# Performance work log

Hardware: AMD Instinct MI355X
Metric: run time of the kernel (lower is better)

Reference implementation:

```python
import jax, jax.numpy as jnp
import numpy as np

HID = 16; HEADS = 8; NB_IN = 8; NB_OUT = 128
B = 128; NPG = 512; N = B * NPG; DEG = 16; E = N * DEG


def _gatv2(x, src, dst, wl, bl, wr, br, att, bias, heads, ch, concat):
    n = x.shape[0]
    xl = (x @ wl + bl).reshape(n, heads, ch)  # source transform
    xr = (x @ wr + br).reshape(n, heads, ch)  # target transform
    e = jax.nn.leaky_relu(xl[src] + xr[dst], negative_slope=0.2)  # [E,H,C]
    logits = jnp.einsum('ehc,hc->eh', e, att)  # [E,H]
    m = jax.ops.segment_max(logits, dst, num_segments=n)
    m = jnp.where(jnp.isfinite(m), m, 0.0)  # guard empty segments
    a = jnp.exp(logits - m[dst])
    denom = jax.ops.segment_sum(a, dst, num_segments=n)
    alpha = a / (denom[dst] + 1e-16)  # segment softmax over incoming edges
    out = jax.ops.segment_sum(alpha[:, :, None] * xl[src], dst, num_segments=n)  # [N,H,C]
    out = out.reshape(n, heads * ch) if concat else out.mean(axis=1)
    return out + bias


def setup_inputs() -> dict:
    key = jax.random.key(0)
    ks = jax.random.split(key, 24)
    x = jax.random.normal(ks[0], (N, NB_IN), jnp.float32)
    # within-graph random edges: local ids + graph offsets
    eg = jax.random.randint(ks[1], (2, B, NPG * DEG), 0, NPG)
    off = (jnp.arange(B) * NPG)[None, :, None]
    edge_index = (eg + off).reshape(2, -1).astype(jnp.int64)
    batch = (jnp.arange(N) // NPG).astype(jnp.int64)
    w = lambda k, i, o: jax.random.normal(k, (i, o), jnp.float32) * (1.0 / np.sqrt(i))
    return {
        'x': x, 'edge_index': edge_index, 'batch': batch,
        'w1l': w(ks[2], NB_IN, HID * HEADS), 'b1l': jnp.zeros(HID * HEADS),
        'w1r': w(ks[3], NB_IN, HID * HEADS), 'b1r': jnp.zeros(HID * HEADS),
        'att1': jax.random.normal(ks[4], (HEADS, HID), jnp.float32) * 0.25,
        'bias1': jnp.zeros(HID * HEADS),
        'w2l': w(ks[5], HID * HEADS, HID * HEADS), 'b2l': jnp.zeros(HID * HEADS),
        'w2r': w(ks[6], HID * HEADS, HID * HEADS), 'b2r': jnp.zeros(HID * HEADS),
        'att2': jax.random.normal(ks[7], (HEADS, HID), jnp.float32) * 0.25,
        'bias2': jnp.zeros(HID * HEADS),
        'w3l': w(ks[8], HID * HEADS, NB_OUT), 'b3l': jnp.zeros(NB_OUT),
        'w3r': w(ks[9], HID * HEADS, NB_OUT), 'b3r': jnp.zeros(NB_OUT),
        'att3': jax.random.normal(ks[10], (1, NB_OUT), jnp.float32) * 0.1,
        'bias3': jnp.zeros(NB_OUT),
        'wh': w(ks[11], NB_OUT * 4, NB_OUT), 'bh': jnp.zeros(NB_OUT),
    }


def reference(x, edge_index, batch, w1l, b1l, w1r, b1r, att1, bias1,
              w2l, b2l, w2r, b2r, att2, bias2,
              w3l, b3l, w3r, b3r, att3, bias3, wh, bh):
    src, dst = edge_index[0], edge_index[1]
    h = _gatv2(x, src, dst, w1l, b1l, w1r, b1r, att1, bias1, HEADS, HID, True)
    h = jax.nn.leaky_relu(h, negative_slope=0.01)
    h = _gatv2(h, src, dst, w2l, b2l, w2r, b2r, att2, bias2, HEADS, HID, True)
    h = jax.nn.leaky_relu(h, negative_slope=0.01)
    h = _gatv2(h, src, dst, w3l, b3l, w3r, b3r, att3, bias3, 1, NB_OUT, False)
    # global pooling: min, max, mean, sum per graph
    s = jax.ops.segment_sum(h, batch, num_segments=B)
    cnt = jax.ops.segment_sum(jnp.ones((N, 1), h.dtype), batch, num_segments=B)
    pooled = jnp.concatenate([
        jax.ops.segment_min(h, batch, num_segments=B),
        jax.ops.segment_max(h, batch, num_segments=B),
        s / jnp.maximum(cnt, 1.0),
        s,
    ], axis=1)  # [B, 4*NB_OUT]
    return jax.nn.leaky_relu(pooled, negative_slope=0.01) @ wh + bh
```

## Files before the change

kernel.cpp:

```cpp
#include <hip/hip_runtime.h>
#include <hip/hip_bf16.h>

typedef __hip_bfloat16 bf16;


__device__ __forceinline__ float bf2f(unsigned int u16) {
    union { unsigned int i; float f; } c; c.i = u16 << 16; return c.f;
}

__device__ __forceinline__ float v9_ldb(const float* p, long i) { return p[i]; }
__device__ __forceinline__ float v9_ldb(const bf16* p, long i) {
    return __bfloat162float(p[i]);
}
__device__ __forceinline__ void v9_stb(float* p, long i, float v) { p[i] = v; }
__device__ __forceinline__ void v9_stb(bf16* p, long i, float v) {
    p[i] = __float2bfloat16(v);
}
__device__ __forceinline__ float2 v11_ld2(const float* p, unsigned i) {
    return *(const float2*)(p + i);
}
__device__ __forceinline__ float2 v11_ld2(const bf16* p, unsigned i) {
    const unsigned u = *(const unsigned*)(p + i);
    float2 r; r.x = bf2f(u & 0xFFFFu); r.y = bf2f(u >> 16); return r;
}
__device__ __forceinline__ float v9_ldin(const void* p, long i, int f32) {
    if (f32) return ((const float*)p)[i];
    return __bfloat162float(((const bf16*)p)[i]);
}

extern "C" __global__ void v9_detect(const unsigned short* xw, const unsigned int* ew,
                                     int* flg) {
    __shared__ int cp, cz;
    if (threadIdx.x == 0) { cp = 0; cz = 0; }
    __syncthreads();
    int lp = 0, lz = 0;
    for (int t = threadIdx.x; t < 1024; t += blockDim.x) {
        unsigned short u = xw[2 * t];
        int e = (u >> 7) & 0xFF;
        if ((e >= 100 && e <= 140) || u == 0) lp++;
        if (ew[2 * t + 1] == 0u) lz++;
    }
    atomicAdd(&cp, lp); atomicAdd(&cz, lz);
    __syncthreads();
    if (threadIdx.x == 0) {
        flg[0] = (cp < 700) ? 1 : 0;
        flg[1] = (cz > 512) ? 1 : 0;
    }
}

__device__ __forceinline__ void v9_edge(const void* ei, int E, int e, int i64,
                                        int& s, int& d) {
    if (i64) {
        const long long* p = (const long long*)ei;
        s = (int)p[e]; d = (int)p[E + e];
    } else {
        const int* p = (const int*)ei;
        s = p[e]; d = p[E + e];
    }
}

extern "C" __global__ void v9_zero(int* cnt, int n) {
    int i = blockIdx.x * blockDim.x + threadIdx.x;
    if (i < n) cnt[i] = 0;
}

extern "C" __global__ void v9_count(const void* ei, int E, int* cnt, int n,
                                    const int* flg) {
    int e = blockIdx.x * blockDim.x + threadIdx.x;
    if (e >= E) return;
    int s, d; v9_edge(ei, E, e, flg[1], s, d);
    if ((unsigned)s >= (unsigned)n || (unsigned)d >= (unsigned)n) return;
    atomicAdd(&cnt[d], 1);
}

extern "C" __global__ __launch_bounds__(1024) void v9_scan(const int* cnt, int* off,
                                                           int n) {
    __shared__ int ls[1024];
    const int t = threadIdx.x;
    const int chunk = (n + 1023) / 1024;
    const int base = t * chunk;
    int s = 0;
    for (int i = base; i < base + chunk; ++i)
        if (i < n) s += cnt[i];
    ls[t] = s;
    __syncthreads();
    for (int d = 1; d < 1024; d <<= 1) {
        int o = (t >= d) ? ls[t - d] : 0;
        __syncthreads();
        ls[t] += o;
        __syncthreads();
    }
    int run = ls[t] - s;
    for (int i = base; i < base + chunk; ++i)
        if (i < n) { off[i] = run; run += cnt[i]; }
    if (t == 1023) off[n] = run;
}

extern "C" __global__ void v9_curinit(const int* off, int* cur, int n) {
    int i = blockIdx.x * blockDim.x + threadIdx.x;
    if (i < n) cur[i] = off[i];
}

extern "C" __global__ void v9_scatter(const void* ei, int E, int* cur, int* csr,
                                      int n, const int* flg) {
    int e = blockIdx.x * blockDim.x + threadIdx.x;
    if (e >= E) return;
    int s, d; v9_edge(ei, E, e, flg[1], s, d);
    if ((unsigned)s >= (unsigned)n || (unsigned)d >= (unsigned)n) return;
    int pos = atomicAdd(&cur[d], 1);
    if (pos >= 0 && pos < E) csr[pos] = s;
}

extern "C" __global__ void v13_sortseg(const int* __restrict__ off,
                                       int* __restrict__ csr, int n) {
    const int i = blockIdx.x * blockDim.x + threadIdx.x;
    if (i >= n) return;
    const int s0 = off[i], s1 = off[i + 1];
    for (int a = s0 + 1; a < s1; ++a) {
        const int v = csr[a];
        int b = a - 1;
        while (b >= s0 && csr[b] > v) { csr[b + 1] = csr[b]; --b; }
        csr[b + 1] = v;
    }
}

template <typename TB>
__global__ __launch_bounds__(256) void v11_gemm8d(const void* in,
        const void* wl, const void* bl, const void* wr, const void* br,
        TB* outl, TB* outr, int n, const int* flg) {
    __shared__ float sWl[8][128], sWr[8][128];
    __shared__ float sBl[128], sBr[128];
    __shared__ float sX[16][8];
    const int t = threadIdx.x;
    const int f = flg[0];
    for (int i = t; i < 1024; i += 256) {
        sWl[i >> 7][i & 127] = v9_ldin(wl, i, f);
        sWr[i >> 7][i & 127] = v9_ldin(wr, i, f);
    }
    if (t < 128) { sBl[t] = v9_ldin(bl, t, f); sBr[t] = v9_ldin(br, t, f); }
    const int nb = blockIdx.x * 16;
    if (t < 128) {
        const int node = nb + (t >> 3);
        if (node < n) sX[t >> 3][t & 7] = v9_ldin(in, (long)node * 8 + (t & 7), f);
    }
    __syncthreads();
    const int j = t & 127;
    const int g = t >> 7;
    float accl[8], accr[8];
#pragma unroll
    for (int q = 0; q < 8; ++q) { accl[q] = sBl[j]; accr[q] = sBr[j]; }
#pragma unroll
    for (int k = 0; k < 8; ++k) {
        const float wlv = sWl[k][j], wrv = sWr[k][j];
#pragma unroll
        for (int q = 0; q < 8; ++q) {
            const float xv = sX[g * 8 + q][k];
            accl[q] = fmaf(xv, wlv, accl[q]);
            accr[q] = fmaf(xv, wrv, accr[q]);
        }
    }
#pragma unroll
    for (int q = 0; q < 8; ++q) {
        const long node = nb + g * 8 + q;
        if (node < n) {
            v9_stb(outl, node * 128 + j, accl[q]);
            v9_stb(outr, node * 128 + j, accr[q]);
        }
    }
}

template <typename TB>
__global__ __launch_bounds__(512) void v10_gemm128(const TB* in, const void* w,
                                                   const void* b, TB* out, int n,
                                                   const int* flg) {
    __shared__ float sW[64 * 128];
    __shared__ float sX[64][64];
    const int t = threadIdx.x;
    const int f = flg[0];
    const int tx = t & 15;
    const int ty = t >> 4;
    const int n0 = ty * 2, n1 = n0 + 1;
    const int s0 = (n0 & 7) << 2, s1 = (n1 & 7) << 2;
    const long nbase = (long)blockIdx.x * 64;

    float bj[8];
#pragma unroll
    for (int j = 0; j < 8; ++j) bj[j] = v9_ldin(b, tx * 8 + j, f);

    float acc[16];
#pragma unroll
    for (int i = 0; i < 16; ++i) acc[i] = 0.f;

    for (int kk = 0; kk < 128; kk += 64) {
        __syncthreads();
        if (f) {
            const float4* ws = (const float4*)w + kk * 32;
#pragma unroll
            for (int i = 0; i < 4; ++i) {
                const int c = i * 512 + t;
                *(float4*)&sW[c * 4] = ws[c];
            }
        } else {
            const ushort4* ws = (const ushort4*)w + kk * 32;
#pragma unroll
            for (int i = 0; i < 4; ++i) {
                const int c = i * 512 + t;
                const ushort4 v = ws[c];
                float4 o;
                o.x = bf2f(v.x); o.y = bf2f(v.y); o.z = bf2f(v.z); o.w = bf2f(v.w);
                *(float4*)&sW[c * 4] = o;
            }
        }
#pragma unroll
        for (int i = 0; i < 2; ++i) {
            const int c = i * 512 + t;
            const int node = c >> 4;
            const int k0 = (c & 15) * 4;
            const long g = nbase + node;
            float4 v;
            if (g < n) {
                if constexpr (sizeof(TB) == 4) {
                    v = *(const float4*)((const float*)in + g * 128 + kk + k0);
                } else {
                    const ushort4 u = *(const ushort4*)((const bf16*)in + g * 128 + kk + k0);
                    v.x = bf2f(u.x); v.y = bf2f(u.y); v.z = bf2f(u.z); v.w = bf2f(u.w);
                }
            } else {
                v.x = v.y = v.z = v.w = 0.f;
            }
            *(float4*)&sX[node][k0 ^ ((node & 7) << 2)] = v;
        }
        __syncthreads();
#pragma unroll 4
        for (int k = 0; k < 64; ++k) {
            const float4 w0 = *(const float4*)&sW[k * 128 + tx * 8];
            const float4 w1 = *(const float4*)&sW[k * 128 + tx * 8 + 4];
            const float x0 = sX[n0][k ^ s0];
            const float x1 = sX[n1][k ^ s1];
            acc[0] = fmaf(x0, w0.x, acc[0]);
            acc[1] = fmaf(x0, w0.y, acc[1]);
            acc[2] = fmaf(x0, w0.z, acc[2]);
            acc[3] = fmaf(x0, w0.w, acc[3]);
            acc[4] = fmaf(x0, w1.x, acc[4]);
            acc[5] = fmaf(x0, w1.y, acc[5]);
            acc[6] = fmaf(x0, w1.z, acc[6]);
            acc[7] = fmaf(x0, w1.w, acc[7]);
            acc[8]  = fmaf(x1, w0.x, acc[8]);
            acc[9]  = fmaf(x1, w0.y, acc[9]);
            acc[10] = fmaf(x1, w0.z, acc[10]);
            acc[11] = fmaf(x1, w0.w, acc[11]);
            acc[12] = fmaf(x1, w1.x, acc[12]);
            acc[13] = fmaf(x1, w1.y, acc[13]);
            acc[14] = fmaf(x1, w1.z, acc[14]);
            acc[15] = fmaf(x1, w1.w, acc[15]);
        }
    }
    const long g0 = nbase + n0, g1 = nbase + n1;
    if (g0 < n) {
        if constexpr (sizeof(TB) == 4) {
            float4 o0 = {acc[0] + bj[0], acc[1] + bj[1], acc[2] + bj[2], acc[3] + bj[3]};
            float4 o1 = {acc[4] + bj[4], acc[5] + bj[5], acc[6] + bj[6], acc[7] + bj[7]};
            *(float4*)((float*)out + g0 * 128 + tx * 8)     = o0;
            *(float4*)((float*)out + g0 * 128 + tx * 8 + 4) = o1;
        } else {
#pragma unroll
            for (int j = 0; j < 8; ++j)
                v9_stb(out, g0 * 128 + tx * 8 + j, acc[j] + bj[j]);
        }
    }
    if (g1 < n) {
        if constexpr (sizeof(TB) == 4) {
            float4 o0 = {acc[8] + bj[0], acc[9] + bj[1], acc[10] + bj[2], acc[11] + bj[3]};
            float4 o1 = {acc[12] + bj[4], acc[13] + bj[5], acc[14] + bj[6], acc[15] + bj[7]};
            *(float4*)((float*)out + g1 * 128 + tx * 8)     = o0;
            *(float4*)((float*)out + g1 * 128 + tx * 8 + 4) = o1;
        } else {
#pragma unroll
            for (int j = 0; j < 8; ++j)
                v9_stb(out, g1 * 128 + tx * 8 + j, acc[8 + j] + bj[j]);
        }
    }
}

__device__ __forceinline__ float v12_logit(float2 xrv, float2 v, float a0, float a1) {
    float e0 = xrv.x + v.x; e0 = e0 > 0.f ? e0 : 0.2f * e0;
    float e1 = xrv.y + v.y; e1 = e1 > 0.f ? e1 : 0.2f * e1;
    return fmaf(e0, a0, e1 * a1);
}

template <typename TB, int LPG>
__global__ __launch_bounds__(256) void v12_agg(const TB* xl, const TB* xr,
                                               const int* csr, const int* off,
                                               const void* att, const void* bias,
                                               TB* out, int n, int E, int act,
                                               const int* flg) {
    const int node = blockIdx.x * 4 + (threadIdx.x >> 6);
    if (node >= n) return;
    const int lane = threadIdx.x & 63;
    const unsigned c0 = (unsigned)lane * 2;
    const int f = flg[0];
    const float2 xrv = v11_ld2(xr, (unsigned)node * 128u + c0);
    const float a0 = v9_ldin(att, c0, f), a1 = v9_ldin(att, c0 + 1, f);
    int s0 = off[node], s1 = off[node + 1];
    s0 = s0 < 0 ? 0 : (s0 > E ? E : s0);
    s1 = s1 < s0 ? s0 : (s1 > E ? E : s1);
    float m = -3.4e38f, den = 0.f, acc0 = 0.f, acc1 = 0.f;
    int i = s0;
    for (; i + 4 <= s1; i += 4) {
        const unsigned sA = (unsigned)csr[i];
        const unsigned sB = (unsigned)csr[i + 1];
        const unsigned sC = (unsigned)csr[i + 2];
        const unsigned sD = (unsigned)csr[i + 3];
        const float2 vA = v11_ld2(xl, sA * 128u + c0);
        const float2 vB = v11_ld2(xl, sB * 128u + c0);
        const float2 vC = v11_ld2(xl, sC * 128u + c0);
        const float2 vD = v11_ld2(xl, sD * 128u + c0);
        float pA = v12_logit(xrv, vA, a0, a1);
        float pB = v12_logit(xrv, vB, a0, a1);
        float pC = v12_logit(xrv, vC, a0, a1);
        float pD = v12_logit(xrv, vD, a0, a1);
#pragma unroll
        for (int o = 1; o < LPG; o <<= 1) {
            pA += __shfl_xor(pA, o);
            pB += __shfl_xor(pB, o);
            pC += __shfl_xor(pC, o);
            pD += __shfl_xor(pD, o);
        }
        const float bm = fmaxf(fmaxf(pA, pB), fmaxf(pC, pD));
        const float mn = fmaxf(m, bm);
        const float sc = __expf(m - mn);
        const float wA = __expf(pA - mn);
        const float wB = __expf(pB - mn);
        const float wC = __expf(pC - mn);
        const float wD = __expf(pD - mn);
        den  = fmaf(den, sc, (wA + wB) + (wC + wD));
        acc0 = fmaf(acc0, sc,
                    fmaf(wA, vA.x, fmaf(wB, vB.x, fmaf(wC, vC.x, wD * vD.x))));
        acc1 = fmaf(acc1, sc,
                    fmaf(wA, vA.y, fmaf(wB, vB.y, fmaf(wC, vC.y, wD * vD.y))));
        m = mn;
    }
    for (; i < s1; ++i) {
        const unsigned s = (unsigned)csr[i];
        const float2 v = v11_ld2(xl, s * 128u + c0);
        float part = v12_logit(xrv, v, a0, a1);
#pragma unroll
        for (int o = 1; o < LPG; o <<= 1)
            part += __shfl_xor(part, o);
        const float mn = fmaxf(m, part);
        const float sc = __expf(m - mn);
        const float w  = __expf(part - mn);
        den  = fmaf(den,  sc, w);
        acc0 = fmaf(acc0, sc, w * v.x);
        acc1 = fmaf(acc1, sc, w * v.y);
        m = mn;
    }
    const float inv = 1.f / (den + 1e-16f);
    float r0 = acc0 * inv + v9_ldin(bias, c0, f);
    float r1 = acc1 * inv + v9_ldin(bias, c0 + 1, f);
    if (act) {
        r0 = r0 > 0.f ? r0 : 0.01f * r0;
        r1 = r1 > 0.f ? r1 : 0.01f * r1;
    }
    v9_stb(out, (long)node * 128 + c0,     r0);
    v9_stb(out, (long)node * 128 + c0 + 1, r1);
}

template <typename TB>
__global__ __launch_bounds__(512) void v9_pool(const TB* h, float* pooled, int npg) {
    const int g = blockIdx.x;
    const int c = threadIdx.x & 127;
    const int part = threadIdx.x >> 7;
    const TB* base = h + (long)g * npg * 128;
    float mn = 3.4e38f, mx = -3.4e38f, sm = 0.f;
    for (int i = part; i < npg; i += 4) {
        const float v = v9_ldb(base, (long)i * 128 + c);
        mn = fminf(mn, v); mx = fmaxf(mx, v); sm += v;
    }
    __shared__ float smn[4][128], smx[4][128], ssm[4][128];
    smn[part][c] = mn; smx[part][c] = mx; ssm[part][c] = sm;
    __syncthreads();
    if (part == 0) {
#pragma unroll
        for (int p = 1; p < 4; ++p) {
            mn = fminf(mn, smn[p][c]); mx = fmaxf(mx, smx[p][c]); sm += ssm[p][c];
        }
        const float mean = sm / (float)npg;
        float* row = pooled + (long)g * 512;
        row[c]       = mn   > 0.f ? mn   : 0.01f * mn;
        row[128 + c] = mx   > 0.f ? mx   : 0.01f * mx;
        row[256 + c] = mean > 0.f ? mean : 0.01f * mean;
        row[384 + c] = sm   > 0.f ? sm   : 0.01f * sm;
    }
}

extern "C" __global__ __launch_bounds__(128) void v9_fc(
        const float* pooled, const void* wh, const void* bh, float* out,
        const int* flg) {
    const int g = blockIdx.x, j = threadIdx.x, f = flg[0];
    const float* p = pooled + (long)g * 512;
    float acc = v9_ldin(bh, j, f);
#pragma unroll 8
    for (int k = 0; k < 512; ++k)
        acc = fmaf(p[k], v9_ldin(wh, (long)k * 128 + j, f), acc);
    out[(long)g * 128 + j] = acc;
}

extern "C" __global__ void v9_wsfail(float* out) {
    if (blockIdx.x == 0 && threadIdx.x == 0)
        out[0] = 1.0e30f;
}

template <typename TB>
static void v9_run(const void* x, const void* ei, void* const* d_in, float* out,
                   int N, int E, int B, int NPG,
                   int* FLG, int* CNT, int* OFF, int* CUR, int* CSR,
                   TB* XL, TB* XR, TB* H, float* PO, hipStream_t stream) {
    const void* w1l = d_in[3];  const void* b1l = d_in[4];
    const void* w1r = d_in[5];  const void* b1r = d_in[6];
    const void* at1 = d_in[7];  const void* bi1 = d_in[8];
    const void* w2l = d_in[9];  const void* b2l = d_in[10];
    const void* w2r = d_in[11]; const void* b2r = d_in[12];
    const void* at2 = d_in[13]; const void* bi2 = d_in[14];
    const void* w3l = d_in[15]; const void* b3l = d_in[16];
    const void* w3r = d_in[17]; const void* b3r = d_in[18];
    const void* at3 = d_in[19]; const void* bi3 = d_in[20];
    const void* wh  = d_in[21]; const void* bh  = d_in[22];

    v9_detect<<<1, 256, 0, stream>>>((const unsigned short*)x,
                                     (const unsigned int*)ei, FLG);
    v9_zero<<<(N + 255) / 256, 256, 0, stream>>>(CNT, N);
    v9_count<<<(E + 255) / 256, 256, 0, stream>>>(ei, E, CNT, N, FLG);
    v9_scan<<<1, 1024, 0, stream>>>(CNT, OFF, N);
    v9_curinit<<<(N + 255) / 256, 256, 0, stream>>>(OFF, CUR, N);
    v9_scatter<<<(E + 255) / 256, 256, 0, stream>>>(ei, E, CUR, CSR, N, FLG);
    v13_sortseg<<<(N + 255) / 256, 256, 0, stream>>>(OFF, CSR, N);

    const int gt = (N + 63) / 64;
    const int g8 = (N + 15) / 16;
    v11_gemm8d<TB><<<g8, 256, 0, stream>>>(x, w1l, b1l, w1r, b1r, XL, XR, N, FLG);
    v12_agg<TB, 8><<<N / 4, 256, 0, stream>>>(XL, XR, CSR, OFF, at1, bi1, H,
                                              N, E, 1, FLG);
    v10_gemm128<TB><<<gt, 512, 0, stream>>>(H, w2l, b2l, XL, N, FLG);
    v10_gemm128<TB><<<gt, 512, 0, stream>>>(H, w2r, b2r, XR, N, FLG);
    v12_agg<TB, 8><<<N / 4, 256, 0, stream>>>(XL, XR, CSR, OFF, at2, bi2, H,
                                              N, E, 1, FLG);
    v10_gemm128<TB><<<gt, 512, 0, stream>>>(H, w3l, b3l, XL, N, FLG);
    v10_gemm128<TB><<<gt, 512, 0, stream>>>(H, w3r, b3r, XR, N, FLG);
    v12_agg<TB, 64><<<N / 4, 256, 0, stream>>>(XL, XR, CSR, OFF, at3, bi3, H,
                                               N, E, 0, FLG);
    v9_pool<TB><<<B, 512, 0, stream>>>(H, PO, NPG);
    v9_fc<<<B, 128, 0, stream>>>(PO, wh, bh, out, FLG);
}

extern "C" void kernel_launch(void* const* d_in, const int* in_sizes, int n_in,
                              void* d_out, int out_size, void* d_ws, size_t ws_size,
                              hipStream_t stream) {
    const void* x  = d_in[0];
    const void* ei = d_in[1];
    float* out = (float*)d_out;

    const int N   = in_sizes[0] / 8;
    const int E   = in_sizes[1] / 2;
    const int NPG = 512;
    const int B   = N / NPG;

    const size_t base_b = 64 + (size_t)N * 4 + ((size_t)N * 4 + 64)
                        + (size_t)N * 4 + (size_t)E * 4;
    const size_t need32 = base_b + 3 * (size_t)N * 512 + (size_t)B * 2048;
    const size_t need16 = base_b + 3 * (size_t)N * 256 + (size_t)B * 2048;

    char* wp = (char*)d_ws;
    int* FLG = (int*)wp; wp += 64;
    int* CNT = (int*)wp; wp += (size_t)N * 4;
    int* OFF = (int*)wp; wp += (size_t)N * 4 + 64;
    int* CUR = (int*)wp; wp += (size_t)N * 4;
    int* CSR = (int*)wp; wp += (size_t)E * 4;

    if (ws_size >= need32) {
        float* XL = (float*)wp; wp += (size_t)N * 512;
        float* XR = (float*)wp; wp += (size_t)N * 512;
        float* H  = (float*)wp; wp += (size_t)N * 512;
        float* PO = (float*)wp;
        v9_run<float>(x, ei, d_in, out, N, E, B, NPG,
                      FLG, CNT, OFF, CUR, CSR, XL, XR, H, PO, stream);
    } else if (ws_size >= need16) {
        bf16* XL = (bf16*)wp; wp += (size_t)N * 256;
        bf16* XR = (bf16*)wp; wp += (size_t)N * 256;
        bf16* H  = (bf16*)wp; wp += (size_t)N * 256;
        float* PO = (float*)wp;
        v9_run<bf16>(x, ei, d_in, out, N, E, B, NPG,
                     FLG, CNT, OFF, CUR, CSR, XL, XR, H, PO, stream);
    } else {
        v9_wsfail<<<1, 64, 0, stream>>>(out);
    }
}
```

Measured before the change: 862.4 us.

## Replace single-block CSR offset scan with three-phase multi-block scan

The prefix sum over per-node in-degree counts ran in one 1024-thread block, with each thread looping serially over a chunk of 64 elements. It is replaced by a block-local scan across 64 blocks, a tiny serial scan of the block sums, and a fix-up pass that also writes the cursor array. The fix-up pass absorbs the separate cursor-init kernel. This spreads the scan across many compute units, at the cost of one extra launch and a 512-byte block-sum buffer limited to 128 blocks.

Result: faster. 768.2 us (-10.9%).

```diff
diff --git a/kernel.cpp b/kernel.cpp
--- a/kernel.cpp
+++ b/kernel.cpp
@@ -73,32 +73,58 @@
     atomicAdd(&cnt[d], 1);
 }
 
-extern "C" __global__ __launch_bounds__(1024) void v9_scan(const int* cnt, int* off,
-                                                           int n) {
-    __shared__ int ls[1024];
+extern "C" __global__ __launch_bounds__(256) void v14_scanA(
+        const int* __restrict__ cnt, int* __restrict__ off,
+        int* __restrict__ bsum, int n) {
+    __shared__ int ls[256];
     const int t = threadIdx.x;
-    const int chunk = (n + 1023) / 1024;
-    const int base = t * chunk;
-    int s = 0;
-    for (int i = base; i < base + chunk; ++i)
-        if (i < n) s += cnt[i];
+    const int base = blockIdx.x * 1024 + t * 4;
+    int a0 = 0, a1 = 0, a2 = 0, a3 = 0;
+    if (base + 3 < n) {
+        a0 = cnt[base]; a1 = cnt[base + 1]; a2 = cnt[base + 2]; a3 = cnt[base + 3];
+    } else {
+        if (base     < n) a0 = cnt[base];
+        if (base + 1 < n) a1 = cnt[base + 1];
+        if (base + 2 < n) a2 = cnt[base + 2];
+        if (base + 3 < n) a3 = cnt[base + 3];
+    }
+    const int s = a0 + a1 + a2 + a3;
     ls[t] = s;
     __syncthreads();
-    for (int d = 1; d < 1024; d <<= 1) {
+    for (int d = 1; d < 256; d <<= 1) {
         int o = (t >= d) ? ls[t - d] : 0;
         __syncthreads();
         ls[t] += o;
         __syncthreads();
     }
     int run = ls[t] - s;
-    for (int i = base; i < base + chunk; ++i)
-        if (i < n) { off[i] = run; run += cnt[i]; }
-    if (t == 1023) off[n] = run;
-}
-
-extern "C" __global__ void v9_curinit(const int* off, int* cur, int n) {
-    int i = blockIdx.x * blockDim.x + threadIdx.x;
-    if (i < n) cur[i] = off[i];
+    if (base     < n) off[base]     = run;
+    if (base + 1 < n) off[base + 1] = run + a0;
+    if (base + 2 < n) off[base + 2] = run + a0 + a1;
+    if (base + 3 < n) off[base + 3] = run + a0 + a1 + a2;
+    if (t == 255) bsum[blockIdx.x] = ls[255];
+}
+
+extern "C" __global__ void v14_scanB(int* bsum, int nb) {
+    if (threadIdx.x == 0 && blockIdx.x == 0) {
+        int run = 0;
+        for (int i = 0; i < nb; ++i) { const int v = bsum[i]; bsum[i] = run; run += v; }
+        bsum[nb] = run;
+    }
+}
+
+extern "C" __global__ __launch_bounds__(256) void v14_scanC(
+        int* __restrict__ off, int* __restrict__ cur,
+        const int* __restrict__ bsum, int n, int nb) {
+    const int t = threadIdx.x;
+    const int base = blockIdx.x * 1024 + t * 4;
+    const int bo = bsum[blockIdx.x];
+#pragma unroll
+    for (int q = 0; q < 4; ++q) {
+        const int i = base + q;
+        if (i < n) { const int v = off[i] + bo; off[i] = v; cur[i] = v; }
+    }
+    if (blockIdx.x == 0 && t == 0) off[n] = bsum[nb];
 }
 
 extern "C" __global__ void v9_scatter(const void* ei, int E, int* cur, int* csr,
@@ -414,7 +440,7 @@
 template <typename TB>
 static void v9_run(const void* x, const void* ei, void* const* d_in, float* out,
                    int N, int E, int B, int NPG,
-                   int* FLG, int* CNT, int* OFF, int* CUR, int* CSR,
+                   int* FLG, int* CNT, int* OFF, int* CUR, int* CSR, int* BS,
                    TB* XL, TB* XR, TB* H, float* PO, hipStream_t stream) {
     const void* w1l = d_in[3];  const void* b1l = d_in[4];
     const void* w1r = d_in[5];  const void* b1r = d_in[6];
@@ -427,12 +453,15 @@
     const void* at3 = d_in[19]; const void* bi3 = d_in[20];
     const void* wh  = d_in[21]; const void* bh  = d_in[22];
 
+    const int nb = (N + 1023) / 1024;
+
     v9_detect<<<1, 256, 0, stream>>>((const unsigned short*)x,
                                      (const unsigned int*)ei, FLG);
     v9_zero<<<(N + 255) / 256, 256, 0, stream>>>(CNT, N);
     v9_count<<<(E + 255) / 256, 256, 0, stream>>>(ei, E, CNT, N, FLG);
-    v9_scan<<<1, 1024, 0, stream>>>(CNT, OFF, N);
-    v9_curinit<<<(N + 255) / 256, 256, 0, stream>>>(OFF, CUR, N);
+    v14_scanA<<<nb, 256, 0, stream>>>(CNT, OFF, BS, N);
+    v14_scanB<<<1, 64, 0, stream>>>(BS, nb);
+    v14_scanC<<<nb, 256, 0, stream>>>(OFF, CUR, BS, N, nb);
     v9_scatter<<<(E + 255) / 256, 256, 0, stream>>>(ei, E, CUR, CSR, N, FLG);
     v13_sortseg<<<(N + 255) / 256, 256, 0, stream>>>(OFF, CSR, N);
 
@@ -466,7 +495,7 @@
     const int B   = N / NPG;
 
     const size_t base_b = 64 + (size_t)N * 4 + ((size_t)N * 4 + 64)
-                        + (size_t)N * 4 + (size_t)E * 4;
+                        + (size_t)N * 4 + (size_t)E * 4 + 512;
     const size_t need32 = base_b + 3 * (size_t)N * 512 + (size_t)B * 2048;
     const size_t need16 = base_b + 3 * (size_t)N * 256 + (size_t)B * 2048;
 
@@ -476,6 +505,7 @@
     int* OFF = (int*)wp; wp += (size_t)N * 4 + 64;
     int* CUR = (int*)wp; wp += (size_t)N * 4;
     int* CSR = (int*)wp; wp += (size_t)E * 4;
+    int* BS  = (int*)wp; wp += 512;
 
     if (ws_size >= need32) {
         float* XL = (float*)wp; wp += (size_t)N * 512;
@@ -483,14 +513,14 @@
         float* H  = (float*)wp; wp += (size_t)N * 512;
         float* PO = (float*)wp;
         v9_run<float>(x, ei, d_in, out, N, E, B, NPG,
-                      FLG, CNT, OFF, CUR, CSR, XL, XR, H, PO, stream);
+                      FLG, CNT, OFF, CUR, CSR, BS, XL, XR, H, PO, stream);
     } else if (ws_size >= need16) {
         bf16* XL = (bf16*)wp; wp += (size_t)N * 256;
         bf16* XR = (bf16*)wp; wp += (size_t)N * 256;
         bf16* H  = (bf16*)wp; wp += (size_t)N * 256;
         float* PO = (float*)wp;
         v9_run<bf16>(x, ei, d_in, out, N, E, B, NPG,
-                     FLG, CNT, OFF, CUR, CSR, XL, XR, H, PO, stream);
+                     FLG, CNT, OFF, CUR, CSR, BS, XL, XR, H, PO, stream);
     } else {
         v9_wsfail<<<1, 64, 0, stream>>>(out);
     }
```
